# Kernel tuning notes

Hardware: AMD Instinct MI355X
Metric: run time of the kernel (lower is better)

## Reference

```python
import jax, jax.numpy as jnp
import numpy as np
from jax import lax

D = 512        # datapathSize (= slow-net hidden size = embedding size)
H = 20         # nonlinearAfterSlowHiddenSize
V = 32000      # softmaxOutputHeadSize = xEmbeddingsNum
T = 1024       # sequence length (number of sequential fast-weight updates)


def setup_inputs() -> dict:
    key = jax.random.key(0)
    ks = jax.random.split(key, 12)
    inp = {}
    inp["tokens"] = jax.random.randint(ks[0], (T,), 0, V)
    inp["targets"] = jax.random.randint(ks[1], (T,), 0, V)
    # learned parameters
    inp["embed"] = jax.random.normal(ks[2], (V, D), dtype=jnp.float32)
    # fastWeightsInit = rand(D,D) * (1/D)
    inp["fw_init"] = jax.random.uniform(ks[3], (D, D), dtype=jnp.float32) * (1.0 / D)
    inp["eta"] = jnp.array(1.0, dtype=jnp.float32)
    inp["wa"] = jax.random.normal(ks[4], (D, D), dtype=jnp.float32) * 0.05
    inp["wb"] = jax.random.normal(ks[5], (D, D), dtype=jnp.float32) * 0.05
    # nonlinearAfterSlow: Linear(D,H) -> selu -> Linear(H,D); stored as (in,out)
    lim_a = 1.0 / np.sqrt(D)
    inp["mlp_aw"] = jax.random.uniform(ks[6], (D, H), dtype=jnp.float32, minval=-lim_a, maxval=lim_a)
    inp["mlp_ab"] = jax.random.uniform(ks[7], (H,), dtype=jnp.float32, minval=-lim_a, maxval=lim_a)
    lim_b = 1.0 / np.sqrt(H)
    inp["mlp_bw"] = jax.random.uniform(ks[8], (H, D), dtype=jnp.float32, minval=-lim_b, maxval=lim_b)
    inp["mlp_bb"] = jax.random.uniform(ks[9], (D,), dtype=jnp.float32, minval=-lim_b, maxval=lim_b)
    # logit head Linear(D, V)
    inp["head_w"] = jax.random.uniform(ks[10], (D, V), dtype=jnp.float32, minval=-lim_a, maxval=lim_a)
    inp["head_b"] = jax.random.uniform(ks[11], (V,), dtype=jnp.float32, minval=-lim_a, maxval=lim_a)
    return inp


def reference(tokens, targets, embed, fw_init, eta, wa, wb,
              mlp_aw, mlp_ab, mlp_bw, mlp_bb, head_w, head_b):
    xs = embed[tokens]  # [T, D]

    def step(fw, x):
        # SlowNetB.forwardAndUpdate for one token
        z0 = x @ wa                      # [D]
        z1 = x @ wb                      # [D]
        fw_new = jnp.tanh(fw + eta * jnp.outer(z0, z1))  # [D, D]
        y = x @ fw_new                   # [D]
        return fw_new, y

    _, ys = lax.scan(step, fw_init, xs)  # ys: [T, D]

    # NonlinearLayer (batched over T)
    h = jax.nn.selu(ys @ mlp_aw + mlp_ab) @ mlp_bw + mlp_bb  # [T, D]
    mixed = 0.5 * h + 0.5 * xs
    logits = mixed @ head_w + head_b     # [T, V]

    logp = jax.nn.log_softmax(logits, axis=-1)
    loss = -jnp.mean(jnp.take_along_axis(logp, targets[:, None], axis=1))
    return logits, loss
```

## Files before the change

kernel.cpp:

```cpp
#include <hip/hip_runtime.h>

#define D 512
#define H 20
#define HP 32
#define V 32000
#define T 1024

typedef unsigned int uint;
typedef __attribute__((ext_vector_type(8))) short short8;
typedef __attribute__((ext_vector_type(4))) float floatx4;

__device__ __forceinline__ unsigned short f2bf(float f) {
    unsigned u = __builtin_bit_cast(unsigned, f);
    u += 0x7fffu + ((u >> 16) & 1u);
    return (unsigned short)(u >> 16);
}

__device__ __forceinline__ float tanh_fast(float x) {
    float t = __builtin_amdgcn_exp2f(x * 2.8853900817779268f);
    float r = __builtin_amdgcn_rcpf(t + 1.0f);
    return __builtin_fmaf(-2.0f, r, 1.0f);
}

template <int CTRL>
__device__ __forceinline__ float dpp_add(float v) {
    int x = __builtin_amdgcn_update_dpp(0, __builtin_bit_cast(int, v), CTRL, 0xf, 0xf, true);
    return v + __builtin_bit_cast(float, x);
}
__device__ __forceinline__ float reduce16(float v) {
    v = dpp_add<0xB1>(v);
    v = dpp_add<0x4E>(v);
    v = dpp_add<0x141>(v);
    v = dpp_add<0x140>(v);
    return v;
}

__global__ __launch_bounds__(256) void gather_kernel(const int* __restrict__ tokens,
                                                     const float* __restrict__ embed,
                                                     float* __restrict__ xs) {
    int idx = blockIdx.x * 256 + threadIdx.x;
    int row = idx >> 7;
    int c   = idx & 127;
    float4 v = ((const float4*)(embed + (long)tokens[row] * D))[c];
    ((float4*)xs)[idx] = v;
}

__global__ __launch_bounds__(256) void zgemm_kernel(const float* __restrict__ xs,
                                                    const float* __restrict__ wa,
                                                    const float* __restrict__ wb,
                                                    float* __restrict__ z0,
                                                    float* __restrict__ z1) {
    __shared__ float Xs[16 * 68];
    __shared__ float Ws[16 * 68];
    const int tid = threadIdx.x;
    const int n0 = blockIdx.x * 64, m0 = blockIdx.y * 64;
    const float* Wm = blockIdx.z ? wb : wa;
    float* Z = blockIdx.z ? z1 : z0;
    const int tx = tid & 15, ty = tid >> 4;
    const int xrow = tid >> 2, xkc = (tid & 3) * 4;
    const int wrow = tid >> 4, wc = (tid & 15) * 4;
    float acc[4][4] = {};
    for (int k0 = 0; k0 < D; k0 += 16) {
        float4 xv = *(const float4*)(xs + (long)(m0 + xrow) * D + k0 + xkc);
        float4 wv = *(const float4*)(Wm + (long)(k0 + wrow) * D + n0 + wc);
        Xs[(xkc + 0) * 68 + xrow] = xv.x;
        Xs[(xkc + 1) * 68 + xrow] = xv.y;
        Xs[(xkc + 2) * 68 + xrow] = xv.z;
        Xs[(xkc + 3) * 68 + xrow] = xv.w;
        *(float4*)(Ws + wrow * 68 + wc) = wv;
        __syncthreads();
#pragma unroll
        for (int k = 0; k < 16; k++) {
            float4 a = *(const float4*)(Xs + k * 68 + ty * 4);
            float4 b = *(const float4*)(Ws + k * 68 + tx * 4);
            float av[4] = {a.x, a.y, a.z, a.w};
            float bv[4] = {b.x, b.y, b.z, b.w};
#pragma unroll
            for (int r = 0; r < 4; r++)
#pragma unroll
                for (int c = 0; c < 4; c++)
                    acc[r][c] = __builtin_fmaf(av[r], bv[c], acc[r][c]);
        }
        __syncthreads();
    }
#pragma unroll
    for (int r = 0; r < 4; r++) {
        float4 v = {acc[r][0], acc[r][1], acc[r][2], acc[r][3]};
        *(float4*)(Z + (long)(m0 + ty * 4 + r) * D + n0 + tx * 4) = v;
    }
}

__global__ __launch_bounds__(256) void scan_kernel(const float* __restrict__ z0,
                                                   const float* __restrict__ z1,
                                                   const float* __restrict__ xs,
                                                   const float* __restrict__ fw_init,
                                                   const float* __restrict__ eta_p,
                                                   float* __restrict__ y) {
    const int tid = threadIdx.x;
    const int j = blockIdx.x;
    const float eta = *eta_p;
    __shared__ float part2[2][8 * 16];
    float f0 = fw_init[(long)tid * D + j];
    float f1 = fw_init[(long)(tid + 256) * D + j];
    float za[8], zb[8], xa[8], xb[8], ez[8];
#pragma unroll
    for (int c = 0; c < 8; c++) {
        const long tr = (long)c * D;
        za[c] = z0[tr + tid];
        zb[c] = z0[tr + tid + 256];
        xa[c] = xs[tr + tid];
        xb[c] = xs[tr + tid + 256];
        ez[c] = z1[tr + j];
    }
    int buf = 0;
    for (int t0 = 0; t0 < T; t0 += 8) {
        float p[8];
#pragma unroll
        for (int c = 0; c < 8; c++) {
            float e = eta * ez[c];
            f0 = tanh_fast(__builtin_fmaf(e, za[c], f0));
            f1 = tanh_fast(__builtin_fmaf(e, zb[c], f1));
            p[c] = xa[c] * f0 + xb[c] * f1;
        }
        if (t0 + 8 < T) {
#pragma unroll
            for (int c = 0; c < 8; c++) {
                const long tr = (long)(t0 + 8 + c) * D;
                za[c] = z0[tr + tid];
                zb[c] = z0[tr + tid + 256];
                xa[c] = xs[tr + tid];
                xb[c] = xs[tr + tid + 256];
                ez[c] = z1[tr + j];
            }
        }
#pragma unroll
        for (int c = 0; c < 8; c++) p[c] = reduce16(p[c]);
        if ((tid & 15) == 0) {
            const int iiH = tid >> 4;
#pragma unroll
            for (int c = 0; c < 8; c++) part2[buf][c * 16 + iiH] = p[c];
        }
        __syncthreads();
        if (tid < 128) {
            const int c = tid >> 4, h = tid & 15;
            float v = part2[buf][c * 16 + h];
            v = reduce16(v);
            if (h == 0) y[(long)(t0 + c) * D + j] = v;
        }
        buf ^= 1;
    }
}

__global__ __launch_bounds__(256) void mlp_a_kernel(const float* __restrict__ y,
                                                    const float* __restrict__ Aw,
                                                    const float* __restrict__ Ab,
                                                    float* __restrict__ hbuf) {
    const int gid = blockIdx.x * 256 + threadIdx.x;
    const int t = gid >> 5, jj = gid & 31;
    if (jj >= H) return;
    float a = 0.f;
    const float* yr = y + (long)t * D;
#pragma unroll 4
    for (int d = 0; d < D; d++) a = __builtin_fmaf(yr[d], Aw[d * H + jj], a);
    a += Ab[jj];
    const float sc = 1.0507009873554805f, al = 1.6732632423543772f;
    hbuf[t * HP + jj] = a > 0.f ? sc * a : sc * al * (__expf(a) - 1.f);
}

__global__ __launch_bounds__(256) void mlp_b_kernel(const float* __restrict__ hbuf,
                                                    const float* __restrict__ xs,
                                                    const float* __restrict__ Bw,
                                                    const float* __restrict__ Bb,
                                                    unsigned short* __restrict__ mixed) {
    const int gid = blockIdx.x * 256 + threadIdx.x;
    const int t = gid >> 9, d = gid & 511;
    float o = Bb[d];
    const float* hr = hbuf + (long)t * HP;
#pragma unroll
    for (int jj = 0; jj < H; jj++) o = __builtin_fmaf(hr[jj], Bw[jj * D + d], o);
    mixed[gid] = f2bf(0.5f * o + 0.5f * xs[gid]);
}

__global__ __launch_bounds__(256) void convert_wt_kernel(const float* __restrict__ head_w,
                                                         unsigned short* __restrict__ wt) {
    __shared__ float tile[64 * 68];
    const int n0 = blockIdx.x * 64, k0 = blockIdx.y * 64;
    const int tid = threadIdx.x;
#pragma unroll
    for (int s = 0; s < 4; s++) {
        int idx4 = s * 256 + tid;
        int r = idx4 >> 4, c4 = idx4 & 15;
        float4 v = *(const float4*)(head_w + (long)(k0 + r) * V + n0 + c4 * 4);
        *(float4*)(tile + r * 68 + c4 * 4) = v;
    }
    __syncthreads();
    const int rr = tid >> 2;
    const int cq = tid & 3;
    uint u[8];
#pragma unroll
    for (int p = 0; p < 8; p++) {
        float a = tile[(cq * 16 + p * 2 + 0) * 68 + rr];
        float b = tile[(cq * 16 + p * 2 + 1) * 68 + rr];
        u[p] = (uint)f2bf(a) | ((uint)f2bf(b) << 16);
    }
    unsigned short* ob = wt + (long)(n0 + rr) * D + k0 + cq * 16;
    uint4 v0 = {u[0], u[1], u[2], u[3]};
    uint4 v1 = {u[4], u[5], u[6], u[7]};
    *(uint4*)ob = v0;
    *((uint4*)ob + 1) = v1;
}

__global__ __launch_bounds__(256) void head_gemm_kernel(const unsigned short* __restrict__ A,
                                                        const unsigned short* __restrict__ Bt,
                                                        const float* __restrict__ bias,
                                                        float* __restrict__ C) {
    __shared__ unsigned short As[128 * 64];
    __shared__ unsigned short Bs[128 * 64];
    const int tid = threadIdx.x;
    const int mt = blockIdx.x & 7, nt = blockIdx.x >> 3;
    const int m0 = mt * 128, n0 = nt * 128;
    const int wave = tid >> 6, lane = tid & 63;
    const int wm = wave >> 1, wn = wave & 1;
    const int quad = lane >> 4, l15 = lane & 15;
    floatx4 acc[4][4] = {};
    for (int k0 = 0; k0 < D; k0 += 64) {
#pragma unroll
        for (int s = 0; s < 4; s++) {
            int idx = s * 256 + tid;
            int row = idx >> 3, slot = idx & 7;
            int gch = slot ^ (row & 7);
            const unsigned short* ga = A + (long)(m0 + row) * D + k0 + gch * 8;
            __builtin_amdgcn_global_load_lds(
                (const __attribute__((address_space(1))) unsigned int*)ga,
                (__attribute__((address_space(3))) unsigned int*)(As + idx * 8), 16, 0, 0);
            const unsigned short* gb = Bt + (long)(n0 + row) * D + k0 + gch * 8;
            __builtin_amdgcn_global_load_lds(
                (const __attribute__((address_space(1))) unsigned int*)gb,
                (__attribute__((address_space(3))) unsigned int*)(Bs + idx * 8), 16, 0, 0);
        }
        __syncthreads();
#pragma unroll
        for (int ks = 0; ks < 2; ks++) {
            short8 af[4], bfr[4];
            int q = ks * 4 + quad;
#pragma unroll
            for (int f = 0; f < 4; f++) {
                int ar = wm * 64 + f * 16 + l15;
                af[f] = *(const short8*)(As + ar * 64 + ((q ^ (ar & 7)) * 8));
                int br = wn * 64 + f * 16 + l15;
                bfr[f] = *(const short8*)(Bs + br * 64 + ((q ^ (br & 7)) * 8));
            }
#pragma unroll
            for (int fr = 0; fr < 4; fr++)
#pragma unroll
                for (int fc = 0; fc < 4; fc++)
                    acc[fr][fc] = __builtin_amdgcn_mfma_f32_16x16x32_bf16(af[fr], bfr[fc],
                                                                          acc[fr][fc], 0, 0, 0);
        }
        __syncthreads();
    }
#pragma unroll
    for (int fc = 0; fc < 4; fc++) {
        int n = n0 + wn * 64 + fc * 16 + l15;
        float b = bias[n];
#pragma unroll
        for (int fr = 0; fr < 4; fr++) {
            int mr = m0 + wm * 64 + fr * 16 + quad * 4;
#pragma unroll
            for (int r = 0; r < 4; r++)
                C[(long)(mr + r) * V + n] = acc[fr][fc][r] + b;
        }
    }
}

__device__ __forceinline__ void lse_upd(float& m, float& s, float v) {
    if (v > m) { s = s * __expf(m - v) + 1.f; m = v; }
    else       { s += __expf(v - m); }
}
__device__ __forceinline__ void lse_comb(float& m, float& s, float m2, float s2) {
    float M = fmaxf(m, m2);
    s = s * __expf(m - M) + s2 * __expf(m2 - M);
    m = M;
}

__global__ __launch_bounds__(256) void loss_rows_kernel(const float* __restrict__ logits,
                                                        const int* __restrict__ targets,
                                                        float* __restrict__ ws_loss) {
    const int t = blockIdx.x, tid = threadIdx.x;
    const float4* row = (const float4*)(logits + (long)t * V);
    float m = -INFINITY, s = 0.f;
    for (int i = tid; i < V / 4; i += 256) {
        float4 v = row[i];
        lse_upd(m, s, v.x); lse_upd(m, s, v.y); lse_upd(m, s, v.z); lse_upd(m, s, v.w);
    }
#pragma unroll
    for (int msk = 1; msk <= 32; msk <<= 1) {
        float m2 = __shfl_xor(m, msk, 64);
        float s2 = __shfl_xor(s, msk, 64);
        lse_comb(m, s, m2, s2);
    }
    __shared__ float sm[4], ss[4];
    if ((tid & 63) == 0) { sm[tid >> 6] = m; ss[tid >> 6] = s; }
    __syncthreads();
    if (tid == 0) {
        float M = sm[0], S = ss[0];
#pragma unroll
        for (int w = 1; w < 4; w++) lse_comb(M, S, sm[w], ss[w]);
        float lse = M + __logf(S);
        float lt = logits[(long)t * V + targets[t]];
        ws_loss[t] = lse - lt;
    }
}

__global__ __launch_bounds__(256) void loss_final_kernel(const float* __restrict__ ws_loss,
                                                         float* __restrict__ out) {
    const int tid = threadIdx.x;
    float s = 0.f;
    for (int i = tid; i < T; i += 256) s += ws_loss[i];
#pragma unroll
    for (int m = 1; m <= 32; m <<= 1) s += __shfl_xor(s, m, 64);
    __shared__ float red[4];
    if ((tid & 63) == 0) red[tid >> 6] = s;
    __syncthreads();
    if (tid == 0) out[0] = (red[0] + red[1] + red[2] + red[3]) * (1.f / (float)T);
}

extern "C" void kernel_launch(void* const* d_in, const int* in_sizes, int n_in,
                              void* d_out, int out_size, void* d_ws, size_t ws_size,
                              hipStream_t stream) {
    const int*   tokens  = (const int*)d_in[0];
    const int*   targets = (const int*)d_in[1];
    const float* embed   = (const float*)d_in[2];
    const float* fw_init = (const float*)d_in[3];
    const float* eta     = (const float*)d_in[4];
    const float* wa      = (const float*)d_in[5];
    const float* wb      = (const float*)d_in[6];
    const float* mlp_aw  = (const float*)d_in[7];
    const float* mlp_ab  = (const float*)d_in[8];
    const float* mlp_bw  = (const float*)d_in[9];
    const float* mlp_bb  = (const float*)d_in[10];
    const float* head_w  = (const float*)d_in[11];
    const float* head_b  = (const float*)d_in[12];
    float* out = (float*)d_out;

    char* ws = (char*)d_ws;
    float*          xs      = (float*)(ws + 0);
    float*          z0      = (float*)(ws + 2097152);
    float*          z1      = (float*)(ws + 4194304);
    float*          y       = (float*)(ws + 6291456);
    unsigned short* mixed   = (unsigned short*)(ws + 8388608);
    unsigned short* wt      = (unsigned short*)(ws + 9437184);
    float*          ws_loss = (float*)(ws + 42205184);
    float*          hbuf    = (float*)(ws + 42209280);

    convert_wt_kernel<<<dim3(V / 64, D / 64), 256, 0, stream>>>(head_w, wt);
    gather_kernel<<<(T * D / 4) / 256, 256, 0, stream>>>(tokens, embed, xs);
    zgemm_kernel<<<dim3(D / 64, T / 64, 2), 256, 0, stream>>>(xs, wa, wb, z0, z1);
    scan_kernel<<<D, 256, 0, stream>>>(z0, z1, xs, fw_init, eta, y);
    mlp_a_kernel<<<(T * HP) / 256, 256, 0, stream>>>(y, mlp_aw, mlp_ab, hbuf);
    mlp_b_kernel<<<(T * D) / 256, 256, 0, stream>>>(hbuf, xs, mlp_bw, mlp_bb, mixed);
    head_gemm_kernel<<<(T / 128) * (V / 128), 256, 0, stream>>>(mixed, wt, head_b, out);
    loss_rows_kernel<<<T, 256, 0, stream>>>(out, targets, ws_loss);
    loss_final_kernel<<<1, 256, 0, stream>>>(ws_loss, out + (long)T * V);
}
```

Before: 567.0 us.

## Fuse softmax partials into head GEMM, widen scan to 512 threads, prescale eta

The head GEMM epilogue now computes per-tile row max and sum-exp partials, so the loss kernel combines 250 partials per row instead of rereading the full 128MB logits matrix. The scan kernel uses 512 threads with one fast-weight element each, doubling per-step parallelism, and eta is folded into the z1 GEMM output. The scan now writes y transposed for the MLP. pm/ps alias the yT buffer, which is safe only because yT is consumed before the head GEMM runs.

Measured after the change: 587.3 us. 1.04x slower.

```diff
diff --git a/kernel.cpp b/kernel.cpp
--- a/kernel.cpp
+++ b/kernel.cpp
@@ -5,6 +5,7 @@
 #define HP 32
 #define V 32000
 #define T 1024
+#define NT 250
 
 typedef unsigned int uint;
 typedef __attribute__((ext_vector_type(8))) short short8;
@@ -23,15 +24,22 @@
 }
 
 template <int CTRL>
-__device__ __forceinline__ float dpp_add(float v) {
+__device__ __forceinline__ float dpp_mov(float v) {
     int x = __builtin_amdgcn_update_dpp(0, __builtin_bit_cast(int, v), CTRL, 0xf, 0xf, true);
-    return v + __builtin_bit_cast(float, x);
+    return __builtin_bit_cast(float, x);
 }
 __device__ __forceinline__ float reduce16(float v) {
-    v = dpp_add<0xB1>(v);
-    v = dpp_add<0x4E>(v);
-    v = dpp_add<0x141>(v);
-    v = dpp_add<0x140>(v);
+    v += dpp_mov<0xB1>(v);
+    v += dpp_mov<0x4E>(v);
+    v += dpp_mov<0x141>(v);
+    v += dpp_mov<0x140>(v);
+    return v;
+}
+__device__ __forceinline__ float redmax16(float v) {
+    v = fmaxf(v, dpp_mov<0xB1>(v));
+    v = fmaxf(v, dpp_mov<0x4E>(v));
+    v = fmaxf(v, dpp_mov<0x141>(v));
+    v = fmaxf(v, dpp_mov<0x140>(v));
     return v;
 }
 
@@ -48,14 +56,16 @@
 __global__ __launch_bounds__(256) void zgemm_kernel(const float* __restrict__ xs,
                                                     const float* __restrict__ wa,
                                                     const float* __restrict__ wb,
+                                                    const float* __restrict__ eta_p,
                                                     float* __restrict__ z0,
-                                                    float* __restrict__ z1) {
+                                                    float* __restrict__ z1s) {
     __shared__ float Xs[16 * 68];
     __shared__ float Ws[16 * 68];
     const int tid = threadIdx.x;
     const int n0 = blockIdx.x * 64, m0 = blockIdx.y * 64;
     const float* Wm = blockIdx.z ? wb : wa;
-    float* Z = blockIdx.z ? z1 : z0;
+    float* Z = blockIdx.z ? z1s : z0;
+    const float scale = blockIdx.z ? *eta_p : 1.0f;
     const int tx = tid & 15, ty = tid >> 4;
     const int xrow = tid >> 2, xkc = (tid & 3) * 4;
     const int wrow = tid >> 4, wc = (tid & 15) * 4;
@@ -85,73 +95,64 @@
     }
 #pragma unroll
     for (int r = 0; r < 4; r++) {
-        float4 v = {acc[r][0], acc[r][1], acc[r][2], acc[r][3]};
+        float4 v = {acc[r][0] * scale, acc[r][1] * scale, acc[r][2] * scale, acc[r][3] * scale};
         *(float4*)(Z + (long)(m0 + ty * 4 + r) * D + n0 + tx * 4) = v;
     }
 }
 
-__global__ __launch_bounds__(256) void scan_kernel(const float* __restrict__ z0,
-                                                   const float* __restrict__ z1,
+__global__ __launch_bounds__(512) void scan_kernel(const float* __restrict__ z0,
+                                                   const float* __restrict__ z1s,
                                                    const float* __restrict__ xs,
                                                    const float* __restrict__ fw_init,
-                                                   const float* __restrict__ eta_p,
-                                                   float* __restrict__ y) {
+                                                   float* __restrict__ yT) {
     const int tid = threadIdx.x;
     const int j = blockIdx.x;
-    const float eta = *eta_p;
-    __shared__ float part2[2][8 * 16];
-    float f0 = fw_init[(long)tid * D + j];
-    float f1 = fw_init[(long)(tid + 256) * D + j];
-    float za[8], zb[8], xa[8], xb[8], ez[8];
+    __shared__ float part2[2][8 * 32];
+    float f = fw_init[(long)tid * D + j];
+    float za[8], xa[8], ez[8];
 #pragma unroll
     for (int c = 0; c < 8; c++) {
         const long tr = (long)c * D;
         za[c] = z0[tr + tid];
-        zb[c] = z0[tr + tid + 256];
         xa[c] = xs[tr + tid];
-        xb[c] = xs[tr + tid + 256];
-        ez[c] = z1[tr + j];
+        ez[c] = z1s[tr + j];
     }
     int buf = 0;
     for (int t0 = 0; t0 < T; t0 += 8) {
         float p[8];
 #pragma unroll
         for (int c = 0; c < 8; c++) {
-            float e = eta * ez[c];
-            f0 = tanh_fast(__builtin_fmaf(e, za[c], f0));
-            f1 = tanh_fast(__builtin_fmaf(e, zb[c], f1));
-            p[c] = xa[c] * f0 + xb[c] * f1;
+            f = tanh_fast(__builtin_fmaf(ez[c], za[c], f));
+            p[c] = xa[c] * f;
         }
         if (t0 + 8 < T) {
 #pragma unroll
             for (int c = 0; c < 8; c++) {
                 const long tr = (long)(t0 + 8 + c) * D;
                 za[c] = z0[tr + tid];
-                zb[c] = z0[tr + tid + 256];
                 xa[c] = xs[tr + tid];
-                xb[c] = xs[tr + tid + 256];
-                ez[c] = z1[tr + j];
+                ez[c] = z1s[tr + j];
             }
         }
 #pragma unroll
         for (int c = 0; c < 8; c++) p[c] = reduce16(p[c]);
         if ((tid & 15) == 0) {
-            const int iiH = tid >> 4;
-#pragma unroll
-            for (int c = 0; c < 8; c++) part2[buf][c * 16 + iiH] = p[c];
+            const int g = tid >> 4;
+#pragma unroll
+            for (int c = 0; c < 8; c++) part2[buf][c * 32 + g] = p[c];
         }
         __syncthreads();
         if (tid < 128) {
             const int c = tid >> 4, h = tid & 15;
-            float v = part2[buf][c * 16 + h];
+            float v = part2[buf][c * 32 + h] + part2[buf][c * 32 + 16 + h];
             v = reduce16(v);
-            if (h == 0) y[(long)(t0 + c) * D + j] = v;
+            if (h == 0) yT[(long)j * T + t0 + c] = v;
         }
         buf ^= 1;
     }
 }
 
-__global__ __launch_bounds__(256) void mlp_a_kernel(const float* __restrict__ y,
+__global__ __launch_bounds__(256) void mlp_a_kernel(const float* __restrict__ yT,
                                                     const float* __restrict__ Aw,
                                                     const float* __restrict__ Ab,
                                                     float* __restrict__ hbuf) {
@@ -159,9 +160,8 @@
     const int t = gid >> 5, jj = gid & 31;
     if (jj >= H) return;
     float a = 0.f;
-    const float* yr = y + (long)t * D;
 #pragma unroll 4
-    for (int d = 0; d < D; d++) a = __builtin_fmaf(yr[d], Aw[d * H + jj], a);
+    for (int d = 0; d < D; d++) a = __builtin_fmaf(yT[(long)d * T + t], Aw[d * H + jj], a);
     a += Ab[jj];
     const float sc = 1.0507009873554805f, al = 1.6732632423543772f;
     hbuf[t * HP + jj] = a > 0.f ? sc * a : sc * al * (__expf(a) - 1.f);
@@ -213,7 +213,9 @@
 __global__ __launch_bounds__(256) void head_gemm_kernel(const unsigned short* __restrict__ A,
                                                         const unsigned short* __restrict__ Bt,
                                                         const float* __restrict__ bias,
-                                                        float* __restrict__ C) {
+                                                        float* __restrict__ C,
+                                                        float* __restrict__ pm,
+                                                        float* __restrict__ ps) {
     __shared__ unsigned short As[128 * 64];
     __shared__ unsigned short Bs[128 * 64];
     const int tid = threadIdx.x;
@@ -259,56 +261,74 @@
         }
         __syncthreads();
     }
+    float bv[4];
+#pragma unroll
+    for (int fc = 0; fc < 4; fc++) bv[fc] = bias[n0 + wn * 64 + fc * 16 + l15];
 #pragma unroll
     for (int fc = 0; fc < 4; fc++) {
         int n = n0 + wn * 64 + fc * 16 + l15;
-        float b = bias[n];
 #pragma unroll
         for (int fr = 0; fr < 4; fr++) {
             int mr = m0 + wm * 64 + fr * 16 + quad * 4;
 #pragma unroll
             for (int r = 0; r < 4; r++)
-                C[(long)(mr + r) * V + n] = acc[fr][fc][r] + b;
-        }
-    }
-}
-
-__device__ __forceinline__ void lse_upd(float& m, float& s, float v) {
-    if (v > m) { s = s * __expf(m - v) + 1.f; m = v; }
-    else       { s += __expf(v - m); }
-}
+                C[(long)(mr + r) * V + n] = acc[fr][fc][r] + bv[fc];
+        }
+    }
+    float* lm = (float*)As;
+    float* lsum = lm + 256;
+#pragma unroll
+    for (int fr = 0; fr < 4; fr++)
+#pragma unroll
+        for (int r = 0; r < 4; r++) {
+            float vm = acc[fr][0][r] + bv[0];
+            vm = fmaxf(vm, acc[fr][1][r] + bv[1]);
+            vm = fmaxf(vm, acc[fr][2][r] + bv[2]);
+            vm = fmaxf(vm, acc[fr][3][r] + bv[3]);
+            vm = redmax16(vm);
+            float vs = 0.f;
+#pragma unroll
+            for (int fc = 0; fc < 4; fc++) vs += __expf(acc[fr][fc][r] + bv[fc] - vm);
+            vs = reduce16(vs);
+            if (l15 == 0) {
+                int row = wm * 64 + fr * 16 + quad * 4 + r;
+                lm[row * 2 + wn] = vm;
+                lsum[row * 2 + wn] = vs;
+            }
+        }
+    __syncthreads();
+    if (tid < 128) {
+        float am = lm[tid * 2 + 0], bm = lm[tid * 2 + 1];
+        float M = fmaxf(am, bm);
+        float S = lsum[tid * 2 + 0] * __expf(am - M) + lsum[tid * 2 + 1] * __expf(bm - M);
+        pm[(long)(m0 + tid) * NT + nt] = M;
+        ps[(long)(m0 + tid) * NT + nt] = S;
+    }
+}
+
 __device__ __forceinline__ void lse_comb(float& m, float& s, float m2, float s2) {
     float M = fmaxf(m, m2);
     s = s * __expf(m - M) + s2 * __expf(m2 - M);
     m = M;
 }
 
-__global__ __launch_bounds__(256) void loss_rows_kernel(const float* __restrict__ logits,
-                                                        const int* __restrict__ targets,
-                                                        float* __restrict__ ws_loss) {
-    const int t = blockIdx.x, tid = threadIdx.x;
-    const float4* row = (const float4*)(logits + (long)t * V);
+__global__ __launch_bounds__(64) void loss_rows_kernel(const float* __restrict__ pm,
+                                                       const float* __restrict__ ps,
+                                                       const float* __restrict__ logits,
+                                                       const int* __restrict__ targets,
+                                                       float* __restrict__ ws_loss) {
+    const int t = blockIdx.x, lane = threadIdx.x;
     float m = -INFINITY, s = 0.f;
-    for (int i = tid; i < V / 4; i += 256) {
-        float4 v = row[i];
-        lse_upd(m, s, v.x); lse_upd(m, s, v.y); lse_upd(m, s, v.z); lse_upd(m, s, v.w);
-    }
+    for (int i = lane; i < NT; i += 64) lse_comb(m, s, pm[(long)t * NT + i], ps[(long)t * NT + i]);
 #pragma unroll
     for (int msk = 1; msk <= 32; msk <<= 1) {
         float m2 = __shfl_xor(m, msk, 64);
         float s2 = __shfl_xor(s, msk, 64);
         lse_comb(m, s, m2, s2);
     }
-    __shared__ float sm[4], ss[4];
-    if ((tid & 63) == 0) { sm[tid >> 6] = m; ss[tid >> 6] = s; }
-    __syncthreads();
-    if (tid == 0) {
-        float M = sm[0], S = ss[0];
-#pragma unroll
-        for (int w = 1; w < 4; w++) lse_comb(M, S, sm[w], ss[w]);
-        float lse = M + __logf(S);
+    if (lane == 0) {
         float lt = logits[(long)t * V + targets[t]];
-        ws_loss[t] = lse - lt;
+        ws_loss[t] = m + __logf(s) - lt;
     }
 }
 
@@ -346,8 +366,10 @@
     char* ws = (char*)d_ws;
     float*          xs      = (float*)(ws + 0);
     float*          z0      = (float*)(ws + 2097152);
-    float*          z1      = (float*)(ws + 4194304);
-    float*          y       = (float*)(ws + 6291456);
+    float*          z1s     = (float*)(ws + 4194304);
+    float*          yT      = (float*)(ws + 6291456);
+    float*          pm      = (float*)(ws + 6291456);
+    float*          ps      = (float*)(ws + 6291456 + 1048576);
     unsigned short* mixed   = (unsigned short*)(ws + 8388608);
     unsigned short* wt      = (unsigned short*)(ws + 9437184);
     float*          ws_loss = (float*)(ws + 42205184);
@@ -355,11 +377,11 @@
 
     convert_wt_kernel<<<dim3(V / 64, D / 64), 256, 0, stream>>>(head_w, wt);
     gather_kernel<<<(T * D / 4) / 256, 256, 0, stream>>>(tokens, embed, xs);
-    zgemm_kernel<<<dim3(D / 64, T / 64, 2), 256, 0, stream>>>(xs, wa, wb, z0, z1);
-    scan_kernel<<<D, 256, 0, stream>>>(z0, z1, xs, fw_init, eta, y);
-    mlp_a_kernel<<<(T * HP) / 256, 256, 0, stream>>>(y, mlp_aw, mlp_ab, hbuf);
+    zgemm_kernel<<<dim3(D / 64, T / 64, 2), 256, 0, stream>>>(xs, wa, wb, eta, z0, z1s);
+    scan_kernel<<<D, 512, 0, stream>>>(z0, z1s, xs, fw_init, yT);
+    mlp_a_kernel<<<(T * HP) / 256, 256, 0, stream>>>(yT, mlp_aw, mlp_ab, hbuf);
     mlp_b_kernel<<<(T * D) / 256, 256, 0, stream>>>(hbuf, xs, mlp_bw, mlp_bb, mixed);
-    head_gemm_kernel<<<(T / 128) * (V / 128), 256, 0, stream>>>(mixed, wt, head_b, out);
-    loss_rows_kernel<<<T, 256, 0, stream>>>(out, targets, ws_loss);
+    head_gemm_kernel<<<(T / 128) * (V / 128), 256, 0, stream>>>(mixed, wt, head_b, out, pm, ps);
+    loss_rows_kernel<<<T, 64, 0, stream>>>(pm, ps, out, targets, ws_loss);
     loss_final_kernel<<<1, 256, 0, stream>>>(ws_loss, out + (long)T * V);
 }
```
